# Optimization experiments

Measured on AMD Instinct MI355X. Metric: run time of the kernel, lower is better.

The kernel has to match this reference:

```python
import jax, jax.numpy as jnp
import numpy as np

N, D, M, L, DEPTH, WIDTH, MPTS = 2048, 64, 2048, 16, 3, 128, 64
WIN = 2 * L + 1  # 33


def setup_inputs() -> dict:
    key = jax.random.key(0)
    ks = jax.random.split(key, 6)
    # xavier-normal-ish scales to keep sigmoids in a reasonable range
    s0 = float(np.sqrt(2.0 / (D + WIDTH)))
    s1 = float(np.sqrt(2.0 / (2 * WIDTH)))
    s2 = float(np.sqrt(2.0 / (WIDTH + WIN)))
    return {
        "u": jax.random.normal(ks[0], (MPTS, D), dtype=jnp.float32),
        "weight0": jax.random.normal(ks[1], (WIN, WIDTH, D), dtype=jnp.float32) * s0,
        "bias0": jnp.zeros((WIN, WIDTH, 1), dtype=jnp.float32),
        "weight": jax.random.normal(ks[2], (DEPTH - 1, WIN, WIDTH, WIDTH), dtype=jnp.float32) * s1,
        "bias": jnp.zeros((DEPTH - 1, WIN, WIDTH, 1), dtype=jnp.float32),
        "weight_final": jax.random.normal(ks[3], (M, WIN, WIDTH), dtype=jnp.float32) * s2,
        "bias_final": jnp.zeros((M, WIN, 1), dtype=jnp.float32),
        "xi": jax.random.normal(ks[4], (M, N + 2 * L), dtype=jnp.float32) * 0.1,
    }


def reference(u, weight0, bias0, weight, bias, weight_final, bias_final, xi):
    sig = jax.nn.sigmoid
    # first_step: shared per-frequency MLP stack
    u1 = sig(jnp.einsum('jkl,ml->jkm', weight0, u) + bias0)
    for i in range(weight.shape[0]):  # depth-1 hidden layers (small fixed count)
        u1 = sig(jnp.einsum('jkl,jlm->jkm', weight[i], u1) + bias[i])
    G = sig(jnp.einsum('ijk,jkm->ijm', weight_final, u1) + bias_final)
    # sliding-window weighted sum over spectral coeffs, vectorized as a 1D
    # cross-correlation: out[n, p] = sum_{m,j} xi[m, n+j] * G[m, j, p]
    kernel = jnp.transpose(G, (2, 0, 1))
    out = jax.lax.conv_general_dilated(
        xi[None],  # [1, M, N+2L]
        kernel,
        window_strides=(1,),
        padding='VALID',
        dimension_numbers=('NCH', 'OIH', 'NCH'),
    )  # [1, MPTS, N]
    return out[0].T  # [N, MPTS] == torch.cat over iter_prod
```

## Files before the change

### kernel.cpp

```cpp
#include <hip/hip_runtime.h>

#define WIN 33
#define WIDTH 128
#define MPTS 64
#define NN 2048
#define MM 2048
#define DD 64
#define NQ 2080

typedef __bf16 bf16x8 __attribute__((ext_vector_type(8)));
typedef float f32x4 __attribute__((ext_vector_type(4)));

__device__ __forceinline__ unsigned short f2bf(float x) {
  union { float f; unsigned int u; } v; v.f = x;
  unsigned int r = v.u + 0x7FFFu + ((v.u >> 16) & 1u);
  return (unsigned short)(r >> 16);
}
__device__ __forceinline__ float sigf(float x) { return 1.0f / (1.0f + __expf(-x)); }

__device__ __forceinline__ void gll16(const unsigned short* g, unsigned short* l) {
  __builtin_amdgcn_global_load_lds(
      (const __attribute__((address_space(1))) unsigned int*)g,
      (__attribute__((address_space(3))) unsigned int*)l, 16, 0, 0);
}

__device__ __forceinline__ bf16x8 cvt8(const float4& a, const float4& b) {
  union { bf16x8 v; unsigned short s[8]; } u;
  u.s[0] = f2bf(a.x); u.s[1] = f2bf(a.y); u.s[2] = f2bf(a.z); u.s[3] = f2bf(a.w);
  u.s[4] = f2bf(b.x); u.s[5] = f2bf(b.y); u.s[6] = f2bf(b.z); u.s[7] = f2bf(b.w);
  return u.v;
}

__global__ __launch_bounds__(256) void k_prep(const float* __restrict__ xi,
                                              unsigned short* __restrict__ xiT,
                                              const float* __restrict__ u,
                                              const float* __restrict__ w0,
                                              const float* __restrict__ b0,
                                              const float* __restrict__ w,
                                              const float* __restrict__ bias,
                                              unsigned short* __restrict__ u1bf,
                                              float* __restrict__ out) {
  extern __shared__ char smem[];
  int bid = blockIdx.x;
  int tid = threadIdx.x;

  if (bid < 33) {
    constexpr int AS = 136;
    float* biass = (float*)smem;
    unsigned short* actA = (unsigned short*)(smem + 1536);
    unsigned short* actB = (unsigned short*)(smem + 18944);
    int j = bid;
    int wv = tid >> 6, lane = tid & 63, l15 = lane & 15, l4 = lane >> 4;
    int colb = l4 << 3;

    const float* wb0 = w + (size_t)j * 16384;
    const float* wb1 = w + (size_t)(WIN + j) * 16384;

    float4 wr0[8], wr1[16], wr2[16];

    {
      float4 ureg[4];
#pragma unroll
      for (int r = 0; r < 4; ++r) {
        int c = tid + (r << 8);
        ureg[r] = *(const float4*)&u[(size_t)(c >> 4) * DD + ((c & 15) << 2)];
      }
#pragma unroll
      for (int s = 0; s < 2; ++s)
#pragma unroll
        for (int t = 0; t < 2; ++t) {
          int row = wv * 32 + s * 16 + l15, col = (t << 5) + colb;
          const float* p = &w0[((size_t)j * 128 + row) * 64 + col];
          wr0[(s * 2 + t) * 2 + 0] = *(const float4*)p;
          wr0[(s * 2 + t) * 2 + 1] = *(const float4*)(p + 4);
        }
#pragma unroll
      for (int s = 0; s < 2; ++s)
#pragma unroll
        for (int t = 0; t < 4; ++t) {
          int row = wv * 32 + s * 16 + l15, col = (t << 5) + colb;
          const float* p = &wb0[(size_t)row * 128 + col];
          wr1[(s * 4 + t) * 2 + 0] = *(const float4*)p;
          wr1[(s * 4 + t) * 2 + 1] = *(const float4*)(p + 4);
        }
      if (tid < 128) {
        biass[tid]       = b0[j * 128 + tid];
        biass[128 + tid] = bias[(size_t)j * 128 + tid];
        biass[256 + tid] = bias[(size_t)(WIN + j) * 128 + tid];
      }
#pragma unroll
      for (int r = 0; r < 4; ++r) {
        int c = tid + (r << 8);
        float4 v = ureg[r];
        ushort4 h; h.x = f2bf(v.x); h.y = f2bf(v.y); h.z = f2bf(v.z); h.w = f2bf(v.w);
        *(ushort4*)&actA[(c >> 4) * AS + ((c & 15) << 2)] = h;
      }
    }
    __syncthreads();

#pragma unroll
    for (int s = 0; s < 2; ++s)
#pragma unroll
      for (int t = 0; t < 4; ++t) {
        int row = wv * 32 + s * 16 + l15, col = (t << 5) + colb;
        const float* p = &wb1[(size_t)row * 128 + col];
        wr2[(s * 4 + t) * 2 + 0] = *(const float4*)p;
        wr2[(s * 4 + t) * 2 + 1] = *(const float4*)(p + 4);
      }
    {
      f32x4 acc[2][4] = {};
#pragma unroll
      for (int t = 0; t < 2; ++t) {
        int col = (t << 5) + colb;
        bf16x8 a[2], b[4];
#pragma unroll
        for (int s = 0; s < 2; ++s)
          a[s] = cvt8(wr0[(s * 2 + t) * 2], wr0[(s * 2 + t) * 2 + 1]);
#pragma unroll
        for (int q = 0; q < 4; ++q)
          b[q] = *(const bf16x8*)&actA[(q * 16 + l15) * AS + col];
#pragma unroll
        for (int s = 0; s < 2; ++s)
#pragma unroll
          for (int q = 0; q < 4; ++q)
            acc[s][q] = __builtin_amdgcn_mfma_f32_16x16x32_bf16(a[s], b[q], acc[s][q], 0, 0, 0);
      }
#pragma unroll
      for (int s = 0; s < 2; ++s)
#pragma unroll
        for (int q = 0; q < 4; ++q) {
          int p = q * 16 + l15;
          int k0 = wv * 32 + s * 16 + (l4 << 2);
          ushort4 st;
          st.x = f2bf(sigf(acc[s][q][0] + biass[k0 + 0]));
          st.y = f2bf(sigf(acc[s][q][1] + biass[k0 + 1]));
          st.z = f2bf(sigf(acc[s][q][2] + biass[k0 + 2]));
          st.w = f2bf(sigf(acc[s][q][3] + biass[k0 + 3]));
          *(ushort4*)&actB[p * AS + k0] = st;
        }
    }
    __syncthreads();

    {
      f32x4 acc[2][4] = {};
#pragma unroll
      for (int t = 0; t < 4; ++t) {
        int col = (t << 5) + colb;
        bf16x8 a[2], b[4];
#pragma unroll
        for (int s = 0; s < 2; ++s)
          a[s] = cvt8(wr1[(s * 4 + t) * 2], wr1[(s * 4 + t) * 2 + 1]);
#pragma unroll
        for (int q = 0; q < 4; ++q)
          b[q] = *(const bf16x8*)&actB[(q * 16 + l15) * AS + col];
#pragma unroll
        for (int s = 0; s < 2; ++s)
#pragma unroll
          for (int q = 0; q < 4; ++q)
            acc[s][q] = __builtin_amdgcn_mfma_f32_16x16x32_bf16(a[s], b[q], acc[s][q], 0, 0, 0);
      }
#pragma unroll
      for (int s = 0; s < 2; ++s)
#pragma unroll
        for (int q = 0; q < 4; ++q) {
          int p = q * 16 + l15;
          int k0 = wv * 32 + s * 16 + (l4 << 2);
          ushort4 st;
          st.x = f2bf(sigf(acc[s][q][0] + biass[128 + k0 + 0]));
          st.y = f2bf(sigf(acc[s][q][1] + biass[128 + k0 + 1]));
          st.z = f2bf(sigf(acc[s][q][2] + biass[128 + k0 + 2]));
          st.w = f2bf(sigf(acc[s][q][3] + biass[128 + k0 + 3]));
          *(ushort4*)&actA[p * AS + k0] = st;
        }
    }
    __syncthreads();

    {
      f32x4 acc[2][4] = {};
#pragma unroll
      for (int t = 0; t < 4; ++t) {
        int col = (t << 5) + colb;
        bf16x8 a[2], b[4];
#pragma unroll
        for (int s = 0; s < 2; ++s)
          a[s] = cvt8(wr2[(s * 4 + t) * 2], wr2[(s * 4 + t) * 2 + 1]);
#pragma unroll
        for (int q = 0; q < 4; ++q)
          b[q] = *(const bf16x8*)&actA[(q * 16 + l15) * AS + col];
#pragma unroll
        for (int s = 0; s < 2; ++s)
#pragma unroll
          for (int q = 0; q < 4; ++q)
            acc[s][q] = __builtin_amdgcn_mfma_f32_16x16x32_bf16(a[s], b[q], acc[s][q], 0, 0, 0);
      }
#pragma unroll
      for (int s = 0; s < 2; ++s)
#pragma unroll
        for (int q = 0; q < 4; ++q) {
          int p = q * 16 + l15;
          int k0 = wv * 32 + s * 16 + (l4 << 2);
          ushort4 st;
          st.x = f2bf(sigf(acc[s][q][0] + biass[256 + k0 + 0]));
          st.y = f2bf(sigf(acc[s][q][1] + biass[256 + k0 + 1]));
          st.z = f2bf(sigf(acc[s][q][2] + biass[256 + k0 + 2]));
          st.w = f2bf(sigf(acc[s][q][3] + biass[256 + k0 + 3]));
          *(ushort4*)&u1bf[((size_t)j * MPTS + p) * WIDTH + k0] = st;
        }
    }
  } else {
    float* ts = (float*)smem;
    int t = bid - 33;
    if (t < 512 && tid < 64) {
      float4 z = {0.f, 0.f, 0.f, 0.f};
      *(float4*)&out[((size_t)t << 8) + (tid << 2)] = z;
    }
    int qt = t % 65, mt = t / 65;
    int qb = qt * 32;
    int mb = mt * 64;
#pragma unroll
    for (int c = tid; c < 512; c += 256) {
      int row = c >> 3, c8 = c & 7;
      float4 v = *(const float4*)&xi[(size_t)(mb + row) * NQ + qb + (c8 << 2)];
      ts[row * 37 + (c8 << 2) + 0] = v.x;
      ts[row * 37 + (c8 << 2) + 1] = v.y;
      ts[row * 37 + (c8 << 2) + 2] = v.z;
      ts[row * 37 + (c8 << 2) + 3] = v.w;
    }
    __syncthreads();
#pragma unroll
    for (int c = tid; c < 512; c += 256) {
      int r = c >> 4, mq = c & 15;
      ushort4 h;
      h.x = f2bf(ts[(mq * 4 + 0) * 37 + r]);
      h.y = f2bf(ts[(mq * 4 + 1) * 37 + r]);
      h.z = f2bf(ts[(mq * 4 + 2) * 37 + r]);
      h.w = f2bf(ts[(mq * 4 + 3) * 37 + r]);
      *(ushort4*)&xiT[((size_t)mt * NQ + (qb + r)) * 64 + (mq << 2)] = h;
    }
  }
}

__global__ __launch_bounds__(256) void k_final(const float* __restrict__ wf,
                                               const float* __restrict__ bfin,
                                               const unsigned short* __restrict__ u1bf,
                                               unsigned short* __restrict__ Gt2) {
  constexpr int KP = 136;
  __shared__ unsigned short As[64 * KP];
  __shared__ unsigned short Bs[64 * KP];
  __shared__ float bfs[64];
  int bid = blockIdx.x;
  int j = bid >> 5;
  int m0 = (bid & 31) << 6;
#pragma unroll
  for (int c = threadIdx.x; c < 64 * 32; c += 256) {
    int row = c >> 5, f4 = c & 31;
    float4 v = *(const float4*)(wf + ((size_t)(m0 + row) * WIN + j) * WIDTH + (f4 << 2));
    ushort4 h;
    h.x = f2bf(v.x); h.y = f2bf(v.y); h.z = f2bf(v.z); h.w = f2bf(v.w);
    *(ushort4*)(&As[row * KP + (f4 << 2)]) = h;
  }
#pragma unroll
  for (int c = threadIdx.x; c < 64 * 16; c += 256) {
    int p = c >> 4, ch = c & 15;
    uint4 v = *(const uint4*)(u1bf + (size_t)(j * MPTS + p) * WIDTH + (ch << 3));
    *(uint4*)(&Bs[p * KP + (ch << 3)]) = v;
  }
  if (threadIdx.x < 64) bfs[threadIdx.x] = bfin[(size_t)(m0 + threadIdx.x) * WIN + j];
  __syncthreads();
  int wv = threadIdx.x >> 6, lane = threadIdx.x & 63;
  int l15 = lane & 15, l4 = lane >> 4;
  f32x4 acc[4] = {};
#pragma unroll
  for (int t = 0; t < 4; ++t) {
    int col = (t << 5) + (l4 << 3);
    bf16x8 a = *(const bf16x8*)(&As[(wv * 16 + l15) * KP + col]);
#pragma unroll
    for (int q = 0; q < 4; ++q) {
      bf16x8 bb = *(const bf16x8*)(&Bs[(q * 16 + l15) * KP + col]);
      acc[q] = __builtin_amdgcn_mfma_f32_16x16x32_bf16(a, bb, acc[q], 0, 0, 0);
    }
  }
  size_t region = (size_t)((bid & 31) << 1) + (wv >> 1);
  int g = ((wv & 1) << 1) + (l4 >> 1);
  int m8 = (l4 & 1) << 2;
  int mb = wv * 16 + (l4 << 2);
#pragma unroll
  for (int q = 0; q < 4; ++q) {
    int p = q * 16 + l15;
    float z0 = acc[q][0] + bfs[mb + 0];
    float z1 = acc[q][1] + bfs[mb + 1];
    float z2 = acc[q][2] + bfs[mb + 2];
    float z3 = acc[q][3] + bfs[mb + 3];
    ushort4 st;
    st.x = f2bf(sigf(z0)); st.y = f2bf(sigf(z1));
    st.z = f2bf(sigf(z2)); st.w = f2bf(sigf(z3));
    *(ushort4*)(&Gt2[region * 67584 + ((size_t)(j * 4 + g) * 64 + p) * 8 + m8]) = st;
  }
}

__global__ __launch_bounds__(256) void k_conv(const unsigned short* __restrict__ xiT,
                                              const unsigned short* __restrict__ Gt2,
                                              float* __restrict__ out) {
  extern __shared__ unsigned short lds[];
  unsigned short* As = lds;
  int bid = blockIdx.x;
  int mp = bid & 31;
  int n0 = (bid >> 5) << 7;
  int tid = threadIdx.x;
  int wv = tid >> 6, lane = tid & 63, l15 = lane & 15, l4 = lane >> 4;

  const unsigned short* Abase = xiT + (size_t)mp * (NQ * 64) + (size_t)n0 * 64;
#pragma unroll
  for (int k = 0; k < 5; ++k) {
    int instr = wv * 5 + k;
    int s = (instr << 6) + lane;
    int row = s >> 3;
    int c = (s & 7) ^ (row & 7);
    gll16(Abase + (size_t)row * 64 + (c << 3), As + (instr << 9));
  }

  constexpr int JBT[10]  = {0, 7, 14, 21, 28, 0, 7, 14, 21, 28};
  constexpr int CNTT[10] = {7, 7, 7, 7, 5, 7, 7, 7, 7, 5};
  constexpr int HFT[10]  = {0, 0, 0, 0, 0, 1, 1, 1, 1, 1};

  const unsigned short* Rb0 = Gt2 + (size_t)(mp << 1) * 67584;
  const unsigned short* Rb1 = Gt2 + (size_t)((mp << 1) + 1) * 67584;

  {
    const unsigned short* Bb = Rb0;
#pragma unroll
    for (int k = 0; k < 7; ++k) {
      int instr = wv * 7 + k;
      gll16(Bb + (((instr << 6) + lane) << 3), lds + 10240 + (instr << 9));
    }
  }

  f32x4 acc[2][4] = {};
#pragma unroll
  for (int t = 0; t < 10; ++t) {
    if (t < 9) {
      const int jbn = JBT[t + 1], cntn = CNTT[t + 1];
      const unsigned short* Bb =
          (HFT[t + 1] ? Rb1 : Rb0) + ((size_t)jbn << 11);
      unsigned short* Bst = lds + 10240 + ((t + 1) & 1) * 14336;
#pragma unroll
      for (int k = 0; k < cntn; ++k) {
        int instr = wv * cntn + k;
        gll16(Bb + (((instr << 6) + lane) << 3), Bst + (instr << 9));
      }
    }
    __builtin_amdgcn_sched_barrier(0);
    if (t == 9)               asm volatile("s_waitcnt vmcnt(0)");
    else if (CNTT[t + 1] == 7) asm volatile("s_waitcnt vmcnt(7)");
    else                       asm volatile("s_waitcnt vmcnt(5)");
    __builtin_amdgcn_sched_barrier(0);
    __builtin_amdgcn_s_barrier();
    {
      const int jb = JBT[t], cnt = CNTT[t], h4 = HFT[t] << 2;
      const unsigned short* Bs = lds + 10240 + (t & 1) * 14336;
      bf16x8 a[2], b[4];
#pragma unroll
      for (int s = 0; s < 2; ++s) {
        int row = wv * 32 + s * 16 + l15 + jb;
        a[s] = *(const bf16x8*)&As[row * 64 + (((h4 | l4) ^ (row & 7)) << 3)];
      }
#pragma unroll
      for (int q = 0; q < 4; ++q) {
        int slot = (l4 << 6) + (q << 4) + l15;
        b[q] = *(const bf16x8*)&Bs[slot << 3];
      }
#pragma unroll
      for (int jj = 0; jj < cnt; ++jj) {
        bf16x8 an[2], bn[4];
        if (jj < cnt - 1) {
#pragma unroll
          for (int s = 0; s < 2; ++s) {
            int row = wv * 32 + s * 16 + l15 + jb + jj + 1;
            an[s] = *(const bf16x8*)&As[row * 64 + (((h4 | l4) ^ (row & 7)) << 3)];
          }
#pragma unroll
          for (int q = 0; q < 4; ++q) {
            int slot = ((((jj + 1) << 2) + l4) << 6) + (q << 4) + l15;
            bn[q] = *(const bf16x8*)&Bs[slot << 3];
          }
        }
#pragma unroll
        for (int s = 0; s < 2; ++s)
#pragma unroll
          for (int q = 0; q < 4; ++q)
            acc[s][q] = __builtin_amdgcn_mfma_f32_16x16x32_bf16(a[s], b[q], acc[s][q], 0, 0, 0);
#pragma unroll
        for (int s = 0; s < 2; ++s) a[s] = an[s];
#pragma unroll
        for (int q = 0; q < 4; ++q) b[q] = bn[q];
      }
    }
    __builtin_amdgcn_s_barrier();
  }
#pragma unroll
  for (int s = 0; s < 2; ++s)
#pragma unroll
    for (int q = 0; q < 4; ++q) {
      int nr = n0 + wv * 32 + s * 16 + (l4 << 2);
      int p = q * 16 + l15;
#pragma unroll
      for (int i = 0; i < 4; ++i)
        atomicAdd(&out[(size_t)(nr + i) * MPTS + p], acc[s][q][i]);
    }
}

extern "C" void kernel_launch(void* const* d_in, const int* in_sizes, int n_in,
                              void* d_out, int out_size, void* d_ws, size_t ws_size,
                              hipStream_t stream) {
  const float* u    = (const float*)d_in[0];
  const float* w0   = (const float*)d_in[1];
  const float* b0   = (const float*)d_in[2];
  const float* w    = (const float*)d_in[3];
  const float* bias = (const float*)d_in[4];
  const float* wf   = (const float*)d_in[5];
  const float* bfin = (const float*)d_in[6];
  const float* xi   = (const float*)d_in[7];
  float* out = (float*)d_out;
  char* ws = (char*)d_ws;
  unsigned short* xiT  = (unsigned short*)(ws);
  unsigned short* Gt2  = (unsigned short*)(ws + 8519680);
  unsigned short* u1bf = (unsigned short*)(ws + 17170432);

  hipFuncSetAttribute(reinterpret_cast<const void*>(&k_prep),
                      hipFuncAttributeMaxDynamicSharedMemorySize, 36352);
  hipFuncSetAttribute(reinterpret_cast<const void*>(&k_conv),
                      hipFuncAttributeMaxDynamicSharedMemorySize, 77824);

  k_prep<<<2113, 256, 36352, stream>>>(xi, xiT, u, w0, b0, w, bias, u1bf, out);
  k_final<<<33 * 32, 256, 0, stream>>>(wf, bfin, u1bf, Gt2);
  k_conv<<<512, 256, 77824, stream>>>(xiT, Gt2, out);
}
```

Baseline: 145.5 us.

## Split conv window taps across wave pairs with 64x64 per-wave tiles

Restructures k_conv so that each pair of waves covers 64 output rows and the two pairs split the window taps (even/odd), instead of every wave owning 32 rows and looping over all taps. Each wave now does a 4x4 MFMA tile, so every loaded A/B fragment feeds more MFMAs. B staging becomes uniform 6-tap chunks over 11 double-buffered stages, which shrinks the LDS footprint. In exchange it uses more accumulator registers, and the duplicated partial sums across tap groups double the atomicAdd traffic to the output.

```diff
diff --git a/kernel.cpp b/kernel.cpp
--- a/kernel.cpp
+++ b/kernel.cpp
@@ -303,11 +303,14 @@
                                               float* __restrict__ out) {
   extern __shared__ unsigned short lds[];
   unsigned short* As = lds;
+  unsigned short* Bb0 = lds + 10240;
   int bid = blockIdx.x;
   int mp = bid & 31;
   int n0 = (bid >> 5) << 7;
   int tid = threadIdx.x;
   int wv = tid >> 6, lane = tid & 63, l15 = lane & 15, l4 = lane >> 4;
+  int wn = wv & 1;
+  int pj = wv >> 1;
 
   const unsigned short* Abase = xiT + (size_t)mp * (NQ * 64) + (size_t)n0 * 64;
 #pragma unroll
@@ -319,93 +322,95 @@
     gll16(Abase + (size_t)row * 64 + (c << 3), As + (instr << 9));
   }
 
-  constexpr int JBT[10]  = {0, 7, 14, 21, 28, 0, 7, 14, 21, 28};
-  constexpr int CNTT[10] = {7, 7, 7, 7, 5, 7, 7, 7, 7, 5};
-  constexpr int HFT[10]  = {0, 0, 0, 0, 0, 1, 1, 1, 1, 1};
-
-  const unsigned short* Rb0 = Gt2 + (size_t)(mp << 1) * 67584;
-  const unsigned short* Rb1 = Gt2 + (size_t)((mp << 1) + 1) * 67584;
-
-  {
-    const unsigned short* Bb = Rb0;
-#pragma unroll
-    for (int k = 0; k < 7; ++k) {
-      int instr = wv * 7 + k;
-      gll16(Bb + (((instr << 6) + lane) << 3), lds + 10240 + (instr << 9));
-    }
-  }
-
-  f32x4 acc[2][4] = {};
-#pragma unroll
-  for (int t = 0; t < 10; ++t) {
-    if (t < 9) {
-      const int jbn = JBT[t + 1], cntn = CNTT[t + 1];
-      const unsigned short* Bb =
-          (HFT[t + 1] ? Rb1 : Rb0) + ((size_t)jbn << 11);
-      unsigned short* Bst = lds + 10240 + ((t + 1) & 1) * 14336;
-#pragma unroll
-      for (int k = 0; k < cntn; ++k) {
-        int instr = wv * cntn + k;
-        gll16(Bb + (((instr << 6) + lane) << 3), Bst + (instr << 9));
+  const unsigned short* Rb = Gt2 + (size_t)(mp << 1) * 67584;
+
+#pragma unroll
+  for (int k = 0; k < 6; ++k) {
+    int i = wv * 6 + k;
+    int uu = i >> 2;
+    const unsigned short* us = Rb + ((size_t)uu << 11);
+    gll16(us + ((i & 3) << 9) + (lane << 3), Bb0 + (i << 9));
+  }
+
+  f32x4 acc[4][4] = {};
+#pragma unroll
+  for (int t = 0; t < 11; ++t) {
+    if (t < 10) {
+#pragma unroll
+      for (int k = 0; k < 6; ++k) {
+        int i = wv * 6 + k;
+        int uu = 6 * (t + 1) + (i >> 2);
+        int hf = (uu >= 33);
+        int jj = uu - (hf ? 33 : 0);
+        const unsigned short* us = Rb + (size_t)hf * 67584 + ((size_t)jj << 11);
+        gll16(us + ((i & 3) << 9) + (lane << 3),
+              Bb0 + ((t + 1) & 1) * 12288 + (i << 9));
       }
     }
     __builtin_amdgcn_sched_barrier(0);
-    if (t == 9)               asm volatile("s_waitcnt vmcnt(0)");
-    else if (CNTT[t + 1] == 7) asm volatile("s_waitcnt vmcnt(7)");
-    else                       asm volatile("s_waitcnt vmcnt(5)");
+    if (t == 10) asm volatile("s_waitcnt vmcnt(0)");
+    else         asm volatile("s_waitcnt vmcnt(6)");
     __builtin_amdgcn_sched_barrier(0);
     __builtin_amdgcn_s_barrier();
+
     {
-      const int jb = JBT[t], cnt = CNTT[t], h4 = HFT[t] << 2;
-      const unsigned short* Bs = lds + 10240 + (t & 1) * 14336;
-      bf16x8 a[2], b[4];
-#pragma unroll
-      for (int s = 0; s < 2; ++s) {
-        int row = wv * 32 + s * 16 + l15 + jb;
-        a[s] = *(const bf16x8*)&As[row * 64 + (((h4 | l4) ^ (row & 7)) << 3)];
-      }
-#pragma unroll
-      for (int q = 0; q < 4; ++q) {
-        int slot = (l4 << 6) + (q << 4) + l15;
-        b[q] = *(const bf16x8*)&Bs[slot << 3];
-      }
-#pragma unroll
-      for (int jj = 0; jj < cnt; ++jj) {
-        bf16x8 an[2], bn[4];
-        if (jj < cnt - 1) {
-#pragma unroll
-          for (int s = 0; s < 2; ++s) {
-            int row = wv * 32 + s * 16 + l15 + jb + jj + 1;
-            an[s] = *(const bf16x8*)&As[row * 64 + (((h4 | l4) ^ (row & 7)) << 3)];
+      const unsigned short* Bs = Bb0 + (t & 1) * 12288;
+      bf16x8 a[4], b[4];
+      {
+        int u0 = 6 * t + pj;
+        int hf = (u0 >= 33);
+        int j0 = u0 - (hf ? 33 : 0);
+        int h4 = hf << 2;
+#pragma unroll
+        for (int g = 0; g < 4; ++g) {
+          int row = wn * 64 + (g << 4) + l15 + j0;
+          a[g] = *(const bf16x8*)&As[row * 64 + (((h4 | l4) ^ (row & 7)) << 3)];
+        }
+#pragma unroll
+        for (int q = 0; q < 4; ++q)
+          b[q] = *(const bf16x8*)&Bs[(size_t)pj * 2048 + (l4 << 9) + (((q << 4) + l15) << 3)];
+      }
+#pragma unroll
+      for (int k = 0; k < 3; ++k) {
+        bf16x8 an[4], bn[4];
+        if (k < 2) {
+          int un = 6 * t + pj + 2 * (k + 1);
+          int hf = (un >= 33);
+          int jn = un - (hf ? 33 : 0);
+          int h4 = hf << 2;
+#pragma unroll
+          for (int g = 0; g < 4; ++g) {
+            int row = wn * 64 + (g << 4) + l15 + jn;
+            an[g] = *(const bf16x8*)&As[row * 64 + (((h4 | l4) ^ (row & 7)) << 3)];
           }
-#pragma unroll
-          for (int q = 0; q < 4; ++q) {
-            int slot = ((((jj + 1) << 2) + l4) << 6) + (q << 4) + l15;
-            bn[q] = *(const bf16x8*)&Bs[slot << 3];
-          }
-        }
-#pragma unroll
-        for (int s = 0; s < 2; ++s)
+          int slot = pj + 2 * (k + 1);
 #pragma unroll
           for (int q = 0; q < 4; ++q)
-            acc[s][q] = __builtin_amdgcn_mfma_f32_16x16x32_bf16(a[s], b[q], acc[s][q], 0, 0, 0);
-#pragma unroll
-        for (int s = 0; s < 2; ++s) a[s] = an[s];
+            bn[q] = *(const bf16x8*)&Bs[(size_t)slot * 2048 + (l4 << 9) + (((q << 4) + l15) << 3)];
+        }
+#pragma unroll
+        for (int g = 0; g < 4; ++g)
+#pragma unroll
+          for (int q = 0; q < 4; ++q)
+            acc[g][q] = __builtin_amdgcn_mfma_f32_16x16x32_bf16(a[g], b[q], acc[g][q], 0, 0, 0);
+#pragma unroll
+        for (int g = 0; g < 4; ++g) a[g] = an[g];
 #pragma unroll
         for (int q = 0; q < 4; ++q) b[q] = bn[q];
       }
     }
     __builtin_amdgcn_s_barrier();
   }
-#pragma unroll
-  for (int s = 0; s < 2; ++s)
+
+#pragma unroll
+  for (int g = 0; g < 4; ++g)
 #pragma unroll
     for (int q = 0; q < 4; ++q) {
-      int nr = n0 + wv * 32 + s * 16 + (l4 << 2);
-      int p = q * 16 + l15;
+      int nr = n0 + wn * 64 + (g << 4) + (l4 << 2);
+      int p = (q << 4) + l15;
 #pragma unroll
       for (int i = 0; i < 4; ++i)
-        atomicAdd(&out[(size_t)(nr + i) * MPTS + p], acc[s][q][i]);
+        atomicAdd(&out[(size_t)(nr + i) * MPTS + p], acc[g][q][i]);
     }
 }
 
@@ -429,9 +434,9 @@
   hipFuncSetAttribute(reinterpret_cast<const void*>(&k_prep),
                       hipFuncAttributeMaxDynamicSharedMemorySize, 36352);
   hipFuncSetAttribute(reinterpret_cast<const void*>(&k_conv),
-                      hipFuncAttributeMaxDynamicSharedMemorySize, 77824);
+                      hipFuncAttributeMaxDynamicSharedMemorySize, 69632);
 
   k_prep<<<2113, 256, 36352, stream>>>(xi, xiT, u, w0, b0, w, bias, u1bf, out);
   k_final<<<33 * 32, 256, 0, stream>>>(wf, bfin, u1bf, Gt2);
-  k_conv<<<512, 256, 77824, stream>>>(xiT, Gt2, out);
-}
+  k_conv<<<512, 256, 69632, stream>>>(xiT, Gt2, out);
+}
```

Result: slower. 166.7 us (+14.6%).
